# Kernel tuning notes

Hardware: AMD Instinct MI355X
Metric: run time of the kernel (lower is better)

## Reference

```python
import jax, jax.numpy as jnp
import numpy as np

WINDOW = (1, 7, 7)
DIM_HEAD = 32


def _rel_pos_index(ws):
    d, h, w = ws
    coords = np.stack(np.meshgrid(np.arange(d), np.arange(h), np.arange(w), indexing='ij'))
    cf = coords.reshape(3, -1)                      # [3, N]
    rel = (cf[:, :, None] - cf[:, None, :]).transpose(1, 2, 0).copy()  # [N, N, 3]
    rel[..., 0] += d - 1
    rel[..., 1] += h - 1
    rel[..., 2] += w - 1
    rel[..., 0] *= (2 * h - 1) * (2 * w - 1)
    rel[..., 1] *= (2 * w - 1)
    return jnp.asarray(rel.sum(-1))                 # [N, N] int32, N = 49


REL_IDX = _rel_pos_index(WINDOW)


def setup_inputs() -> dict:
    key = jax.random.key(0)
    k1, k2, k3, k4, k5 = jax.random.split(key, 5)
    B, X, Y, W1, W2, D = 4, 32, 32, 7, 7, 512
    heads = D // DIM_HEAD
    n_bias = (2 * WINDOW[0] - 1) * (2 * WINDOW[1] - 1) * (2 * WINDOW[2] - 1)  # 169
    s = 1.0 / np.sqrt(D)
    return {
        'x': jax.random.normal(k1, (B, X, Y, W1, W2, D), jnp.float32),
        'y': jax.random.normal(k2, (B, X, Y, W1, W2, D), jnp.float32),
        'Wq': jax.random.normal(k3, (D, D), jnp.float32) * s,
        'Wkv': jax.random.normal(k4, (D, 2 * D), jnp.float32) * s,
        'bias_table': jax.random.normal(k5, (n_bias, heads), jnp.float32) * 0.02,
    }


def reference(x, y, Wq, Wkv, bias_table):
    B, X, Y, W1, W2, D = x.shape
    h = D // DIM_HEAD
    n = W1 * W2                                     # 49 tokens per window
    scale = DIM_HEAD ** -0.5

    xr = x.reshape(B * X * Y, n, D)                 # [Bw, n, D]
    yr = y.reshape(B * X * Y, n, D)

    q = xr @ Wq                                     # [Bw, n, D]
    kv = yr @ Wkv                                   # [Bw, n, 2D]
    k, v = kv[..., :D], kv[..., D:]

    def to_heads(t):
        return t.reshape(t.shape[0], n, h, DIM_HEAD).transpose(0, 2, 1, 3)  # [Bw, h, n, dh]

    q, k, v = to_heads(q), to_heads(k), to_heads(v)

    sim = jnp.einsum('bhid,bhjd->bhij', q, k) * scale   # [Bw, h, n, n]
    bias = bias_table[REL_IDX]                          # [n, n, h]
    sim = sim + bias.transpose(2, 0, 1)[None]           # broadcast over windows

    attn = jax.nn.softmax(sim, axis=-1)
    out = jnp.einsum('bhij,bhjd->bhid', attn, v)        # [Bw, h, n, dh]
    out = out.transpose(0, 2, 1, 3).reshape(B * X * Y, W1, W2, D)
    return out.reshape(B, X, Y, W1, W2, D)
```

## Files before the change

kernel.cpp:

```cpp
#include <hip/hip_runtime.h>


typedef __bf16 bf16x8 __attribute__((ext_vector_type(8)));
typedef __attribute__((ext_vector_type(4))) float f32x4;

#define DEVI __device__ __forceinline__

DEVI unsigned short f2bf(float f) {
  union { float f; unsigned u; } v; v.f = f;
  unsigned r = v.u + 0x7FFFu + ((v.u >> 16) & 1u);
  return (unsigned short)(r >> 16);
}
DEVI unsigned pkbf(float a, float b) {
  return (unsigned)f2bf(a) | ((unsigned)f2bf(b) << 16);
}

#define MFMA16(a, b, c) __builtin_amdgcn_mfma_f32_16x16x32_bf16((a), (b), (c), 0, 0, 0)

#define SWZ_Y(r)  ((((unsigned)(r)) & 7u) << 4)
#define SWZ_A(r)  (((((unsigned)(r)) >> 2) & 3u) << 5)
#define SWZ_P(r)  ((((unsigned)(r)) & 7u) << 4)
#define SWZ_VT(r) ((((unsigned)(r)) & 7u) << 4)

__global__ void prep_kernel(const float* __restrict__ Wq, const float* __restrict__ Wkv,
                            const float* __restrict__ bt, char* __restrict__ ws) {
  int t = blockIdx.x * 256 + threadIdx.x;
  if (t < 786432) {
    int e = t & 7, lane = (t >> 3) & 63, ks = (t >> 9) & 15, nt = (t >> 13) & 1,
        h = (t >> 14) & 15, T = t >> 18;
    int row = ks * 32 + (lane >> 4) * 8 + e;
    int col = h * 32 + nt * 16 + (lane & 15);
    float v;
    if (T == 0)      v = Wq[row * 512 + col] * 0.17677669529663687f;
    else if (T == 1) v = Wkv[row * 1024 + col];
    else             v = Wkv[row * 1024 + 512 + col];
    ((unsigned short*)ws)[t] = f2bf(v);
  }
  if (t < 262144) {
    int r = t & 3, lane = (t >> 2) & 63, nt = (t >> 8) & 3, mt = (t >> 10) & 3,
        h = (t >> 12) & 15;
    int i = mt * 16 + (lane & 15);
    int j = nt * 16 + ((lane >> 4) & 3) * 4 + r;
    float v;
    if (j >= 49)      v = -1e30f;
    else if (i >= 49) v = 0.0f;
    else {
      int hi = i / 7, wi = i % 7, hj = j / 7, wj = j % 7;
      v = bt[((hi - hj + 6) * 13 + (wi - wj + 6)) * 16 + h];
    }
    ((float*)(ws + 1572864))[t] = v;
  }
}

DEVI bf16x8 ldXY(const char* base, int row, int kc) {
  unsigned a = ((unsigned)(row * 1024 + kc * 2)) ^ SWZ_Y(row);
  return *(const bf16x8*)(base + a);
}
DEVI bf16x8 ldXY_c(const char* base, int row, int kc) {
  int rc = row < 48 ? row : 48;
  bf16x8 v = ldXY(base, rc, kc);
  if (row > 48) {
    union { long long z[2]; bf16x8 v; } u; u.z[0] = 0; u.z[1] = 0;
    v = u.v;
  }
  return v;
}
DEVI bf16x8 ldA(const char* base, int row, int kc) {
  int rc = row < 48 ? row : 48;
  unsigned a = ((unsigned)(rc * 64 + kc * 2)) ^ SWZ_A(rc);
  return *(const bf16x8*)(base + a);
}
DEVI bf16x8 ldP2(const char* base, int row, int jc) {
  int rc = row < 48 ? row : 48;
  unsigned a = ((unsigned)(rc * 128 + jc * 2)) ^ SWZ_P(rc);
  return *(const bf16x8*)(base + a);
}
DEVI bf16x8 ldVT(const char* base, int dh, int jc) {
  unsigned a = ((unsigned)(dh * 128 + jc * 2)) ^ SWZ_VT(dh);
  return *(const bf16x8*)(base + a);
}

__global__ __launch_bounds__(512, 2)
void attn_kernel(const float* __restrict__ x, const float* __restrict__ y,
                 const char* __restrict__ wsW, const float* __restrict__ biasD,
                 float* __restrict__ out) {
  extern __shared__ char smem[];
  char* xb = smem;
  char* yb = smem + 50176;
  const int tid = threadIdx.x;
  const int lane = tid & 63, wave = tid >> 6;
  const int p = wave >> 1, sub = wave & 1;
  const int g = lane >> 4, lr = lane & 15;
  char* pbase = smem + 100352 + p * 15872;
  char* qAb = pbase;
  char* kbuf = pbase + 3136;
  char* qBb = pbase + 6272;
  char* vt = pbase + 9408;

  const int bw = blockIdx.x;
  const float* xs = x + (size_t)bw * 25088;
  const float* ys = y + (size_t)bw * 25088;

  for (int it = tid; it < 6272; it += 512) {
    float4 v = ((const float4*)xs)[it];
    float4 w = ((const float4*)ys)[it];
    int i = it >> 7;
    int k = (it & 127) << 2;
    unsigned a = ((unsigned)(i * 1024 + k * 2)) ^ SWZ_Y(i);
    uint2 ux, uy;
    ux.x = pkbf(v.x, v.y); ux.y = pkbf(v.z, v.w);
    uy.x = pkbf(w.x, w.y); uy.y = pkbf(w.z, w.w);
    *(uint2*)(xb + a) = ux;
    *(uint2*)(yb + a) = uy;
  }

  const bf16x8* wsQ = (const bf16x8*)wsW;
  const bf16x8* wsK = (const bf16x8*)(wsW + 524288);
  const bf16x8* wsV = (const bf16x8*)(wsW + 1048576);
  const f32x4* bD = (const f32x4*)biasD;
  const f32x4 fz = {0.f, 0.f, 0.f, 0.f};

  auto storeQK = [&](char* qb, f32x4 (&acc)[4]) {
    #pragma unroll
    for (int mt = 0; mt < 4; ++mt)
      #pragma unroll
      for (int r = 0; r < 4; ++r) {
        int row = mt * 16 + g * 4 + r;
        if (row < 49) {
          unsigned a = ((unsigned)(row * 64 + (sub * 16 + lr) * 2)) ^ SWZ_A(row);
          *(unsigned short*)(qb + a) = f2bf(acc[mt][r]);
        }
      }
  };

  auto kv_compute = [&](int h, f32x4 (&ak)[4], f32x4 (&av)[4]) {
    #pragma unroll
    for (int mt = 0; mt < 4; ++mt) { ak[mt] = fz; av[mt] = fz; }
    const bf16x8* pK = wsK + (size_t)((h * 2 + sub) * 16) * 64 + lane;
    const bf16x8* pV = wsV + (size_t)((h * 2 + sub) * 16) * 64 + lane;
    bf16x8 ksr[8], vsr[8];
    #pragma unroll
    for (int i = 0; i < 8; ++i) { ksr[i] = pK[i * 64]; vsr[i] = pV[i * 64]; }
    #pragma unroll
    for (int ks = 0; ks < 16; ++ks) {
      bf16x8 bk = ksr[ks & 7], bv = vsr[ks & 7];
      if (ks < 8) { ksr[ks & 7] = pK[(ks + 8) * 64]; vsr[ks & 7] = pV[(ks + 8) * 64]; }
      int kc = ks * 32 + g * 8;
      bf16x8 a0 = ldXY(yb, lr, kc);
      bf16x8 a1 = ldXY(yb, lr + 16, kc);
      bf16x8 a2 = ldXY(yb, lr + 32, kc);
      bf16x8 a3 = ldXY_c(yb, lr + 48, kc);
      ak[0] = MFMA16(a0, bk, ak[0]);
      ak[1] = MFMA16(a1, bk, ak[1]);
      ak[2] = MFMA16(a2, bk, ak[2]);
      ak[3] = MFMA16(a3, bk, ak[3]);
      av[0] = MFMA16(a0, bv, av[0]);
      av[1] = MFMA16(a1, bv, av[1]);
      av[2] = MFMA16(a2, bv, av[2]);
      av[3] = MFMA16(a3, bv, av[3]);
    }
  };

  auto kv_store = [&](f32x4 (&ak)[4], f32x4 (&av)[4]) {
    storeQK(kbuf, ak);
    #pragma unroll
    for (int mt = 0; mt < 4; ++mt) {
      int dh = sub * 16 + lr;
      int t0 = mt * 16 + g * 4;
      unsigned a = ((unsigned)(dh * 128 + t0 * 2)) ^ SWZ_VT(dh);
      uint2 pk;
      pk.x = pkbf(av[mt][0], av[mt][1]);
      pk.y = pkbf(av[mt][2], av[mt][3]);
      *(uint2*)(vt + a) = pk;
    }
  };

  auto attn_head = [&](int h, const char* qbuf, char* Pb) {
    f32x4 bias[2][4];
    #pragma unroll
    for (int mi = 0; mi < 2; ++mi)
      #pragma unroll
      for (int nt = 0; nt < 4; ++nt)
        bias[mi][nt] = bD[(size_t)(((h * 4 + sub * 2 + mi) * 4 + nt) * 64 + lane)];

    bf16x8 qa[2], kf[4];
    #pragma unroll
    for (int mi = 0; mi < 2; ++mi) qa[mi] = ldA(qbuf, sub * 32 + mi * 16 + lr, g * 8);
    #pragma unroll
    for (int nt = 0; nt < 4; ++nt) kf[nt] = ldA(kbuf, nt * 16 + lr, g * 8);

    f32x4 accs[2][4];
    #pragma unroll
    for (int mi = 0; mi < 2; ++mi)
      #pragma unroll
      for (int nt = 0; nt < 4; ++nt)
        accs[mi][nt] = MFMA16(kf[nt], qa[mi], fz);

    uint2 pks[2][4];
    #pragma unroll
    for (int mi = 0; mi < 2; ++mi) {
      f32x4 vals[4];
      #pragma unroll
      for (int nt = 0; nt < 4; ++nt) vals[nt] = accs[mi][nt] + bias[mi][nt];
      float m = vals[0][0];
      #pragma unroll
      for (int nt = 0; nt < 4; ++nt)
        #pragma unroll
        for (int r = 0; r < 4; ++r) m = fmaxf(m, vals[nt][r]);
      m = fmaxf(m, __shfl_xor(m, 16));
      m = fmaxf(m, __shfl_xor(m, 32));
      float s = 0.f;
      #pragma unroll
      for (int nt = 0; nt < 4; ++nt)
        #pragma unroll
        for (int r = 0; r < 4; ++r) {
          float pv = __expf(vals[nt][r] - m);
          vals[nt][r] = pv;
          s += pv;
        }
      s += __shfl_xor(s, 16);
      s += __shfl_xor(s, 32);
      float inv = 1.0f / s;
      #pragma unroll
      for (int nt = 0; nt < 4; ++nt) {
        pks[mi][nt].x = pkbf(vals[nt][0] * inv, vals[nt][1] * inv);
        pks[mi][nt].y = pkbf(vals[nt][2] * inv, vals[nt][3] * inv);
      }
    }

    __syncthreads();

    #pragma unroll
    for (int mi = 0; mi < 2; ++mi) {
      int i = sub * 32 + mi * 16 + lr;
      if (i < 49) {
        #pragma unroll
        for (int nt = 0; nt < 4; ++nt) {
          unsigned a = ((unsigned)(i * 128 + (nt * 16 + g * 4) * 2)) ^ SWZ_P(i);
          *(uint2*)(Pb + a) = pks[mi][nt];
        }
      }
    }

    f32x4 acco[2][2];
    acco[0][0] = fz; acco[0][1] = fz; acco[1][0] = fz; acco[1][1] = fz;
    #pragma unroll
    for (int ks = 0; ks < 2; ++ks) {
      int jc = ks * 32 + g * 8;
      bf16x8 av0 = ldVT(vt, lr, jc);
      bf16x8 av1 = ldVT(vt, lr + 16, jc);
      bf16x8 bp0 = ldP2(Pb, sub * 32 + lr, jc);
      bf16x8 bp1 = ldP2(Pb, sub * 32 + 16 + lr, jc);
      acco[0][0] = MFMA16(av0, bp0, acco[0][0]);
      acco[0][1] = MFMA16(av0, bp1, acco[0][1]);
      acco[1][0] = MFMA16(av1, bp0, acco[1][0]);
      acco[1][1] = MFMA16(av1, bp1, acco[1][1]);
    }

    float* ow = out + (size_t)bw * 25088 + h * 32;
    #pragma unroll
    for (int it = 0; it < 2; ++it) {
      int tok = sub * 32 + it * 16 + lr;
      if (tok < 49) {
        #pragma unroll
        for (int dt = 0; dt < 2; ++dt)
          *(f32x4*)(&ow[(size_t)tok * 512 + dt * 16 + g * 4]) = acco[dt][it];
      }
    }
  };

  for (int hp = 0; hp < 2; ++hp) {
    const int hA = p * 4 + hp * 2, hB = hA + 1;

    __syncthreads();

    f32x4 aqA[4], aqB[4];
    #pragma unroll
    for (int mt = 0; mt < 4; ++mt) { aqA[mt] = fz; aqB[mt] = fz; }
    {
      const bf16x8* pQA = wsQ + (size_t)((hA * 2 + sub) * 16) * 64 + lane;
      const bf16x8* pQB = wsQ + (size_t)((hB * 2 + sub) * 16) * 64 + lane;
      bf16x8 ra[8], rb[8];
      #pragma unroll
      for (int i = 0; i < 8; ++i) { ra[i] = pQA[i * 64]; rb[i] = pQB[i * 64]; }
      #pragma unroll
      for (int ks = 0; ks < 16; ++ks) {
        bf16x8 fa = ra[ks & 7], fb = rb[ks & 7];
        if (ks < 8) { ra[ks & 7] = pQA[(ks + 8) * 64]; rb[ks & 7] = pQB[(ks + 8) * 64]; }
        int kc = ks * 32 + g * 8;
        bf16x8 a0 = ldXY(xb, lr, kc);
        bf16x8 a1 = ldXY(xb, lr + 16, kc);
        bf16x8 a2 = ldXY(xb, lr + 32, kc);
        bf16x8 a3 = ldXY_c(xb, lr + 48, kc);
        aqA[0] = MFMA16(a0, fa, aqA[0]);
        aqA[1] = MFMA16(a1, fa, aqA[1]);
        aqA[2] = MFMA16(a2, fa, aqA[2]);
        aqA[3] = MFMA16(a3, fa, aqA[3]);
        aqB[0] = MFMA16(a0, fb, aqB[0]);
        aqB[1] = MFMA16(a1, fb, aqB[1]);
        aqB[2] = MFMA16(a2, fb, aqB[2]);
        aqB[3] = MFMA16(a3, fb, aqB[3]);
      }
    }
    storeQK(qAb, aqA);
    storeQK(qBb, aqB);

    {
      f32x4 ak[4], av[4];
      kv_compute(hA, ak, av);
      kv_store(ak, av);
    }

    __syncthreads();

    attn_head(hA, qAb, pbase);

    {
      f32x4 ak[4], av[4];
      kv_compute(hB, ak, av);
      __syncthreads();
      kv_store(ak, av);
    }

    __syncthreads();

    attn_head(hB, qBb, pbase + 3136);
  }
}

extern "C" void kernel_launch(void* const* d_in, const int* in_sizes, int n_in,
                              void* d_out, int out_size, void* d_ws, size_t ws_size,
                              hipStream_t stream) {
  (void)in_sizes; (void)n_in; (void)out_size; (void)ws_size;
  const float* x = (const float*)d_in[0];
  const float* y = (const float*)d_in[1];
  const float* Wq = (const float*)d_in[2];
  const float* Wkv = (const float*)d_in[3];
  const float* bt = (const float*)d_in[4];
  float* out = (float*)d_out;
  char* ws = (char*)d_ws;

  prep_kernel<<<3072, 256, 0, stream>>>(Wq, Wkv, bt, ws);

  (void)hipFuncSetAttribute((const void*)attn_kernel,
                            hipFuncAttributeMaxDynamicSharedMemorySize, 163840);
  attn_kernel<<<4096, 512, 163840, stream>>>(x, y, (const char*)ws,
                                             (const float*)(ws + 1572864), out);
}
```

Before: 843.2 us.

## Give each wave whole heads and pass Q, V, P through register shuffles

Work is reassigned so each of the eight waves owns two full heads, instead of a pair of waves splitting each head. Q, V and the softmax probabilities are transposed into MFMA operand layout with cross-lane shuffles, not written to and read back from shared memory. Only K goes through a small per-wave scratch area, so the per-head block-wide barriers become wave-local LDS waits and the shared-memory footprint shrinks. The cost is more shuffle instructions, more registers per wave (risking spills at 512 threads with 2 blocks per CU) and roughly twice the weight loads per wave.

```diff
diff --git a/kernel.cpp b/kernel.cpp
--- a/kernel.cpp
+++ b/kernel.cpp
@@ -16,11 +16,11 @@
 }
 
 #define MFMA16(a, b, c) __builtin_amdgcn_mfma_f32_16x16x32_bf16((a), (b), (c), 0, 0, 0)
+#define WAVE_DS_FENCE() do { asm volatile("s_waitcnt lgkmcnt(0)" ::: "memory"); \
+                             __builtin_amdgcn_sched_barrier(0); } while (0)
 
 #define SWZ_Y(r)  ((((unsigned)(r)) & 7u) << 4)
 #define SWZ_A(r)  (((((unsigned)(r)) >> 2) & 3u) << 5)
-#define SWZ_P(r)  ((((unsigned)(r)) & 7u) << 4)
-#define SWZ_VT(r) ((((unsigned)(r)) & 7u) << 4)
 
 __global__ void prep_kernel(const float* __restrict__ Wq, const float* __restrict__ Wkv,
                             const float* __restrict__ bt, char* __restrict__ ws) {
@@ -56,28 +56,32 @@
   unsigned a = ((unsigned)(row * 1024 + kc * 2)) ^ SWZ_Y(row);
   return *(const bf16x8*)(base + a);
 }
-DEVI bf16x8 ldXY_c(const char* base, int row, int kc) {
+DEVI bf16x8 ldXYc(const char* base, int row, int kc) {
   int rc = row < 48 ? row : 48;
-  bf16x8 v = ldXY(base, rc, kc);
-  if (row > 48) {
-    union { long long z[2]; bf16x8 v; } u; u.z[0] = 0; u.z[1] = 0;
-    v = u.v;
-  }
-  return v;
+  return ldXY(base, rc, kc);
 }
 DEVI bf16x8 ldA(const char* base, int row, int kc) {
   int rc = row < 48 ? row : 48;
   unsigned a = ((unsigned)(rc * 64 + kc * 2)) ^ SWZ_A(rc);
   return *(const bf16x8*)(base + a);
 }
-DEVI bf16x8 ldP2(const char* base, int row, int jc) {
-  int rc = row < 48 ? row : 48;
-  unsigned a = ((unsigned)(rc * 128 + jc * 2)) ^ SWZ_P(rc);
-  return *(const bf16x8*)(base + a);
-}
-DEVI bf16x8 ldVT(const char* base, int dh, int jc) {
-  unsigned a = ((unsigned)(dh * 128 + jc * 2)) ^ SWZ_VT(dh);
-  return *(const bf16x8*)(base + a);
+
+DEVI uint2 shfl_u2(uint2 v, int src) {
+  uint2 r;
+  r.x = (unsigned)__shfl((int)v.x, src);
+  r.y = (unsigned)__shfl((int)v.y, src);
+  return r;
+}
+DEVI bf16x8 xfrag(uint2 c0, uint2 c1, int srcA, int srcB, bool hig) {
+  uint2 a0 = shfl_u2(c0, srcA), a1 = shfl_u2(c1, srcA);
+  uint2 b0 = shfl_u2(c0, srcB), b1 = shfl_u2(c1, srcB);
+  uint2 lo = hig ? a1 : a0, hi = hig ? b1 : b0;
+  union { unsigned u[4]; bf16x8 v; } r;
+  r.u[0] = lo.x; r.u[1] = lo.y; r.u[2] = hi.x; r.u[3] = hi.y;
+  return r.v;
+}
+DEVI uint2 pk4(const f32x4& a) {
+  uint2 r; r.x = pkbf(a[0], a[1]); r.y = pkbf(a[2], a[3]); return r;
 }
 
 __global__ __launch_bounds__(512, 2)
@@ -89,13 +93,12 @@
   char* yb = smem + 50176;
   const int tid = threadIdx.x;
   const int lane = tid & 63, wave = tid >> 6;
-  const int p = wave >> 1, sub = wave & 1;
   const int g = lane >> 4, lr = lane & 15;
-  char* pbase = smem + 100352 + p * 15872;
-  char* qAb = pbase;
-  char* kbuf = pbase + 3136;
-  char* qBb = pbase + 6272;
-  char* vt = pbase + 9408;
+  char* kscr = smem + 100352 + wave * 3136;
+
+  const int srcA = lr + ((g & 1) << 5);
+  const int srcB = srcA + 16;
+  const bool hig = g >= 2;
 
   const int bw = blockIdx.x;
   const float* xs = x + (size_t)bw * 25088;
@@ -113,6 +116,7 @@
     *(uint2*)(xb + a) = ux;
     *(uint2*)(yb + a) = uy;
   }
+  __syncthreads();
 
   const bf16x8* wsQ = (const bf16x8*)wsW;
   const bf16x8* wsK = (const bf16x8*)(wsW + 524288);
@@ -120,211 +124,190 @@
   const f32x4* bD = (const f32x4*)biasD;
   const f32x4 fz = {0.f, 0.f, 0.f, 0.f};
 
-  auto storeQK = [&](char* qb, f32x4 (&acc)[4]) {
+  for (int hh = 0; hh < 2; ++hh) {
+    const int h = wave * 2 + hh;
+    WAVE_DS_FENCE();
+
+    f32x4 aQ[2][4];
+    #pragma unroll
+    for (int m = 0; m < 2; ++m)
+      #pragma unroll
+      for (int n = 0; n < 4; ++n) aQ[m][n] = fz;
+    {
+      const bf16x8* pQ0 = wsQ + (size_t)((h * 2 + 0) * 16) * 64 + lane;
+      const bf16x8* pQ1 = wsQ + (size_t)((h * 2 + 1) * 16) * 64 + lane;
+      bf16x8 ra[8], rb[8];
+      #pragma unroll
+      for (int i = 0; i < 8; ++i) { ra[i] = pQ0[i * 64]; rb[i] = pQ1[i * 64]; }
+      #pragma unroll
+      for (int ks = 0; ks < 16; ++ks) {
+        bf16x8 w0 = ra[ks & 7], w1 = rb[ks & 7];
+        if (ks < 8) { ra[ks & 7] = pQ0[(ks + 8) * 64]; rb[ks & 7] = pQ1[(ks + 8) * 64]; }
+        int kc = ks * 32 + g * 8;
+        bf16x8 b0 = ldXY(xb, lr, kc);
+        bf16x8 b1 = ldXY(xb, lr + 16, kc);
+        bf16x8 b2 = ldXY(xb, lr + 32, kc);
+        bf16x8 b3 = ldXYc(xb, lr + 48, kc);
+        aQ[0][0] = MFMA16(w0, b0, aQ[0][0]);
+        aQ[0][1] = MFMA16(w0, b1, aQ[0][1]);
+        aQ[0][2] = MFMA16(w0, b2, aQ[0][2]);
+        aQ[0][3] = MFMA16(w0, b3, aQ[0][3]);
+        aQ[1][0] = MFMA16(w1, b0, aQ[1][0]);
+        aQ[1][1] = MFMA16(w1, b1, aQ[1][1]);
+        aQ[1][2] = MFMA16(w1, b2, aQ[1][2]);
+        aQ[1][3] = MFMA16(w1, b3, aQ[1][3]);
+      }
+    }
+    uint2 pkQ[2][4];
+    #pragma unroll
+    for (int m = 0; m < 2; ++m)
+      #pragma unroll
+      for (int n = 0; n < 4; ++n) pkQ[m][n] = pk4(aQ[m][n]);
+
+    f32x4 aK[4][2], aV[4][2];
+    #pragma unroll
+    for (int mt = 0; mt < 4; ++mt) {
+      aK[mt][0] = fz; aK[mt][1] = fz; aV[mt][0] = fz; aV[mt][1] = fz;
+    }
+    {
+      const bf16x8* pK0 = wsK + (size_t)((h * 2 + 0) * 16) * 64 + lane;
+      const bf16x8* pK1 = wsK + (size_t)((h * 2 + 1) * 16) * 64 + lane;
+      const bf16x8* pV0 = wsV + (size_t)((h * 2 + 0) * 16) * 64 + lane;
+      const bf16x8* pV1 = wsV + (size_t)((h * 2 + 1) * 16) * 64 + lane;
+      bf16x8 rk0[4], rk1[4], rv0[4], rv1[4];
+      #pragma unroll
+      for (int i = 0; i < 4; ++i) {
+        rk0[i] = pK0[i * 64]; rk1[i] = pK1[i * 64];
+        rv0[i] = pV0[i * 64]; rv1[i] = pV1[i * 64];
+      }
+      #pragma unroll
+      for (int ks = 0; ks < 16; ++ks) {
+        bf16x8 k0 = rk0[ks & 3], k1 = rk1[ks & 3];
+        bf16x8 v0 = rv0[ks & 3], v1 = rv1[ks & 3];
+        if (ks < 12) {
+          rk0[ks & 3] = pK0[(ks + 4) * 64]; rk1[ks & 3] = pK1[(ks + 4) * 64];
+          rv0[ks & 3] = pV0[(ks + 4) * 64]; rv1[ks & 3] = pV1[(ks + 4) * 64];
+        }
+        int kc = ks * 32 + g * 8;
+        bf16x8 a0 = ldXY(yb, lr, kc);
+        bf16x8 a1 = ldXY(yb, lr + 16, kc);
+        bf16x8 a2 = ldXY(yb, lr + 32, kc);
+        bf16x8 a3 = ldXYc(yb, lr + 48, kc);
+        aK[0][0] = MFMA16(a0, k0, aK[0][0]);
+        aK[1][0] = MFMA16(a1, k0, aK[1][0]);
+        aK[2][0] = MFMA16(a2, k0, aK[2][0]);
+        aK[3][0] = MFMA16(a3, k0, aK[3][0]);
+        aK[0][1] = MFMA16(a0, k1, aK[0][1]);
+        aK[1][1] = MFMA16(a1, k1, aK[1][1]);
+        aK[2][1] = MFMA16(a2, k1, aK[2][1]);
+        aK[3][1] = MFMA16(a3, k1, aK[3][1]);
+        aV[0][0] = MFMA16(a0, v0, aV[0][0]);
+        aV[1][0] = MFMA16(a1, v0, aV[1][0]);
+        aV[2][0] = MFMA16(a2, v0, aV[2][0]);
+        aV[3][0] = MFMA16(a3, v0, aV[3][0]);
+        aV[0][1] = MFMA16(a0, v1, aV[0][1]);
+        aV[1][1] = MFMA16(a1, v1, aV[1][1]);
+        aV[2][1] = MFMA16(a2, v1, aV[2][1]);
+        aV[3][1] = MFMA16(a3, v1, aV[3][1]);
+      }
+    }
     #pragma unroll
     for (int mt = 0; mt < 4; ++mt)
       #pragma unroll
-      for (int r = 0; r < 4; ++r) {
-        int row = mt * 16 + g * 4 + r;
-        if (row < 49) {
-          unsigned a = ((unsigned)(row * 64 + (sub * 16 + lr) * 2)) ^ SWZ_A(row);
-          *(unsigned short*)(qb + a) = f2bf(acc[mt][r]);
+      for (int nt = 0; nt < 2; ++nt)
+        #pragma unroll
+        for (int r = 0; r < 4; ++r) {
+          int row = mt * 16 + g * 4 + r;
+          if (row < 49) {
+            unsigned a = ((unsigned)(row * 64 + (nt * 16 + lr) * 2)) ^ SWZ_A(row);
+            *(unsigned short*)(kscr + a) = f2bf(aK[mt][nt][r]);
+          }
         }
-      }
-  };
-
-  auto kv_compute = [&](int h, f32x4 (&ak)[4], f32x4 (&av)[4]) {
-    #pragma unroll
-    for (int mt = 0; mt < 4; ++mt) { ak[mt] = fz; av[mt] = fz; }
-    const bf16x8* pK = wsK + (size_t)((h * 2 + sub) * 16) * 64 + lane;
-    const bf16x8* pV = wsV + (size_t)((h * 2 + sub) * 16) * 64 + lane;
-    bf16x8 ksr[8], vsr[8];
-    #pragma unroll
-    for (int i = 0; i < 8; ++i) { ksr[i] = pK[i * 64]; vsr[i] = pV[i * 64]; }
-    #pragma unroll
-    for (int ks = 0; ks < 16; ++ks) {
-      bf16x8 bk = ksr[ks & 7], bv = vsr[ks & 7];
-      if (ks < 8) { ksr[ks & 7] = pK[(ks + 8) * 64]; vsr[ks & 7] = pV[(ks + 8) * 64]; }
-      int kc = ks * 32 + g * 8;
-      bf16x8 a0 = ldXY(yb, lr, kc);
-      bf16x8 a1 = ldXY(yb, lr + 16, kc);
-      bf16x8 a2 = ldXY(yb, lr + 32, kc);
-      bf16x8 a3 = ldXY_c(yb, lr + 48, kc);
-      ak[0] = MFMA16(a0, bk, ak[0]);
-      ak[1] = MFMA16(a1, bk, ak[1]);
-      ak[2] = MFMA16(a2, bk, ak[2]);
-      ak[3] = MFMA16(a3, bk, ak[3]);
-      av[0] = MFMA16(a0, bv, av[0]);
-      av[1] = MFMA16(a1, bv, av[1]);
-      av[2] = MFMA16(a2, bv, av[2]);
-      av[3] = MFMA16(a3, bv, av[3]);
-    }
-  };
-
-  auto kv_store = [&](f32x4 (&ak)[4], f32x4 (&av)[4]) {
-    storeQK(kbuf, ak);
+    uint2 pkV[4][2];
     #pragma unroll
     for (int mt = 0; mt < 4; ++mt) {
-      int dh = sub * 16 + lr;
-      int t0 = mt * 16 + g * 4;
-      unsigned a = ((unsigned)(dh * 128 + t0 * 2)) ^ SWZ_VT(dh);
-      uint2 pk;
-      pk.x = pkbf(av[mt][0], av[mt][1]);
-      pk.y = pkbf(av[mt][2], av[mt][3]);
-      *(uint2*)(vt + a) = pk;
-    }
-  };
-
-  auto attn_head = [&](int h, const char* qbuf, char* Pb) {
-    f32x4 bias[2][4];
-    #pragma unroll
-    for (int mi = 0; mi < 2; ++mi)
-      #pragma unroll
-      for (int nt = 0; nt < 4; ++nt)
-        bias[mi][nt] = bD[(size_t)(((h * 4 + sub * 2 + mi) * 4 + nt) * 64 + lane)];
-
-    bf16x8 qa[2], kf[4];
-    #pragma unroll
-    for (int mi = 0; mi < 2; ++mi) qa[mi] = ldA(qbuf, sub * 32 + mi * 16 + lr, g * 8);
-    #pragma unroll
-    for (int nt = 0; nt < 4; ++nt) kf[nt] = ldA(kbuf, nt * 16 + lr, g * 8);
-
-    f32x4 accs[2][4];
-    #pragma unroll
-    for (int mi = 0; mi < 2; ++mi)
-      #pragma unroll
-      for (int nt = 0; nt < 4; ++nt)
-        accs[mi][nt] = MFMA16(kf[nt], qa[mi], fz);
-
-    uint2 pks[2][4];
-    #pragma unroll
-    for (int mi = 0; mi < 2; ++mi) {
+      pkV[mt][0] = pk4(aV[mt][0]);
+      pkV[mt][1] = pk4(aV[mt][1]);
+    }
+    WAVE_DS_FENCE();
+    bf16x8 kf[4];
+    #pragma unroll
+    for (int jt = 0; jt < 4; ++jt) kf[jt] = ldA(kscr, jt * 16 + lr, g * 8);
+
+    uint2 pkP[4][4];
+    f32x4 bnext[4];
+    #pragma unroll
+    for (int jt = 0; jt < 4; ++jt)
+      bnext[jt] = bD[(size_t)(((h * 4 + 0) * 4 + jt) * 64 + lane)];
+    #pragma unroll
+    for (int it = 0; it < 4; ++it) {
+      f32x4 bs[4];
+      #pragma unroll
+      for (int jt = 0; jt < 4; ++jt) bs[jt] = bnext[jt];
+      if (it < 3) {
+        #pragma unroll
+        for (int jt = 0; jt < 4; ++jt)
+          bnext[jt] = bD[(size_t)(((h * 4 + it + 1) * 4 + jt) * 64 + lane)];
+      }
+      bf16x8 qf = xfrag(pkQ[0][it], pkQ[1][it], srcA, srcB, hig);
       f32x4 vals[4];
       #pragma unroll
-      for (int nt = 0; nt < 4; ++nt) vals[nt] = accs[mi][nt] + bias[mi][nt];
+      for (int jt = 0; jt < 4; ++jt) vals[jt] = MFMA16(kf[jt], qf, fz);
+      #pragma unroll
+      for (int jt = 0; jt < 4; ++jt) vals[jt] = vals[jt] + bs[jt];
       float m = vals[0][0];
       #pragma unroll
-      for (int nt = 0; nt < 4; ++nt)
-        #pragma unroll
-        for (int r = 0; r < 4; ++r) m = fmaxf(m, vals[nt][r]);
+      for (int jt = 0; jt < 4; ++jt)
+        #pragma unroll
+        for (int r = 0; r < 4; ++r) m = fmaxf(m, vals[jt][r]);
       m = fmaxf(m, __shfl_xor(m, 16));
       m = fmaxf(m, __shfl_xor(m, 32));
       float s = 0.f;
       #pragma unroll
-      for (int nt = 0; nt < 4; ++nt)
+      for (int jt = 0; jt < 4; ++jt)
         #pragma unroll
         for (int r = 0; r < 4; ++r) {
-          float pv = __expf(vals[nt][r] - m);
-          vals[nt][r] = pv;
+          float pv = __expf(vals[jt][r] - m);
+          vals[jt][r] = pv;
           s += pv;
         }
       s += __shfl_xor(s, 16);
       s += __shfl_xor(s, 32);
       float inv = 1.0f / s;
       #pragma unroll
-      for (int nt = 0; nt < 4; ++nt) {
-        pks[mi][nt].x = pkbf(vals[nt][0] * inv, vals[nt][1] * inv);
-        pks[mi][nt].y = pkbf(vals[nt][2] * inv, vals[nt][3] * inv);
-      }
-    }
-
-    __syncthreads();
-
-    #pragma unroll
-    for (int mi = 0; mi < 2; ++mi) {
-      int i = sub * 32 + mi * 16 + lr;
-      if (i < 49) {
-        #pragma unroll
-        for (int nt = 0; nt < 4; ++nt) {
-          unsigned a = ((unsigned)(i * 128 + (nt * 16 + g * 4) * 2)) ^ SWZ_P(i);
-          *(uint2*)(Pb + a) = pks[mi][nt];
-        }
-      }
-    }
-
-    f32x4 acco[2][2];
-    acco[0][0] = fz; acco[0][1] = fz; acco[1][0] = fz; acco[1][1] = fz;
+      for (int jt = 0; jt < 4; ++jt) {
+        pkP[it][jt].x = pkbf(vals[jt][0] * inv, vals[jt][1] * inv);
+        pkP[it][jt].y = pkbf(vals[jt][2] * inv, vals[jt][3] * inv);
+      }
+    }
+
+    f32x4 acco[2][4];
+    #pragma unroll
+    for (int md = 0; md < 2; ++md)
+      #pragma unroll
+      for (int it = 0; it < 4; ++it) acco[md][it] = fz;
     #pragma unroll
     for (int ks = 0; ks < 2; ++ks) {
-      int jc = ks * 32 + g * 8;
-      bf16x8 av0 = ldVT(vt, lr, jc);
-      bf16x8 av1 = ldVT(vt, lr + 16, jc);
-      bf16x8 bp0 = ldP2(Pb, sub * 32 + lr, jc);
-      bf16x8 bp1 = ldP2(Pb, sub * 32 + 16 + lr, jc);
-      acco[0][0] = MFMA16(av0, bp0, acco[0][0]);
-      acco[0][1] = MFMA16(av0, bp1, acco[0][1]);
-      acco[1][0] = MFMA16(av1, bp0, acco[1][0]);
-      acco[1][1] = MFMA16(av1, bp1, acco[1][1]);
+      bf16x8 aV0 = xfrag(pkV[ks * 2][0], pkV[ks * 2 + 1][0], srcA, srcB, hig);
+      bf16x8 aV1 = xfrag(pkV[ks * 2][1], pkV[ks * 2 + 1][1], srcA, srcB, hig);
+      #pragma unroll
+      for (int it = 0; it < 4; ++it) {
+        bf16x8 bP = xfrag(pkP[it][ks * 2], pkP[it][ks * 2 + 1], srcA, srcB, hig);
+        acco[0][it] = MFMA16(aV0, bP, acco[0][it]);
+        acco[1][it] = MFMA16(aV1, bP, acco[1][it]);
+      }
     }
 
     float* ow = out + (size_t)bw * 25088 + h * 32;
     #pragma unroll
-    for (int it = 0; it < 2; ++it) {
-      int tok = sub * 32 + it * 16 + lr;
+    for (int it = 0; it < 4; ++it) {
+      int tok = it * 16 + lr;
       if (tok < 49) {
         #pragma unroll
-        for (int dt = 0; dt < 2; ++dt)
-          *(f32x4*)(&ow[(size_t)tok * 512 + dt * 16 + g * 4]) = acco[dt][it];
-      }
-    }
-  };
-
-  for (int hp = 0; hp < 2; ++hp) {
-    const int hA = p * 4 + hp * 2, hB = hA + 1;
-
-    __syncthreads();
-
-    f32x4 aqA[4], aqB[4];
-    #pragma unroll
-    for (int mt = 0; mt < 4; ++mt) { aqA[mt] = fz; aqB[mt] = fz; }
-    {
-      const bf16x8* pQA = wsQ + (size_t)((hA * 2 + sub) * 16) * 64 + lane;
-      const bf16x8* pQB = wsQ + (size_t)((hB * 2 + sub) * 16) * 64 + lane;
-      bf16x8 ra[8], rb[8];
-      #pragma unroll
-      for (int i = 0; i < 8; ++i) { ra[i] = pQA[i * 64]; rb[i] = pQB[i * 64]; }
-      #pragma unroll
-      for (int ks = 0; ks < 16; ++ks) {
-        bf16x8 fa = ra[ks & 7], fb = rb[ks & 7];
-        if (ks < 8) { ra[ks & 7] = pQA[(ks + 8) * 64]; rb[ks & 7] = pQB[(ks + 8) * 64]; }
-        int kc = ks * 32 + g * 8;
-        bf16x8 a0 = ldXY(xb, lr, kc);
-        bf16x8 a1 = ldXY(xb, lr + 16, kc);
-        bf16x8 a2 = ldXY(xb, lr + 32, kc);
-        bf16x8 a3 = ldXY_c(xb, lr + 48, kc);
-        aqA[0] = MFMA16(a0, fa, aqA[0]);
-        aqA[1] = MFMA16(a1, fa, aqA[1]);
-        aqA[2] = MFMA16(a2, fa, aqA[2]);
-        aqA[3] = MFMA16(a3, fa, aqA[3]);
-        aqB[0] = MFMA16(a0, fb, aqB[0]);
-        aqB[1] = MFMA16(a1, fb, aqB[1]);
-        aqB[2] = MFMA16(a2, fb, aqB[2]);
-        aqB[3] = MFMA16(a3, fb, aqB[3]);
-      }
-    }
-    storeQK(qAb, aqA);
-    storeQK(qBb, aqB);
-
-    {
-      f32x4 ak[4], av[4];
-      kv_compute(hA, ak, av);
-      kv_store(ak, av);
-    }
-
-    __syncthreads();
-
-    attn_head(hA, qAb, pbase);
-
-    {
-      f32x4 ak[4], av[4];
-      kv_compute(hB, ak, av);
-      __syncthreads();
-      kv_store(ak, av);
-    }
-
-    __syncthreads();
-
-    attn_head(hB, qBb, pbase + 3136);
+        for (int md = 0; md < 2; ++md)
+          *(f32x4*)(&ow[(size_t)tok * 512 + md * 16 + g * 4]) = acco[md][it];
+      }
+    }
   }
 }
 
@@ -343,7 +326,7 @@
   prep_kernel<<<3072, 256, 0, stream>>>(Wq, Wkv, bt, ws);
 
   (void)hipFuncSetAttribute((const void*)attn_kernel,
-                            hipFuncAttributeMaxDynamicSharedMemorySize, 163840);
-  attn_kernel<<<4096, 512, 163840, stream>>>(x, y, (const char*)ws,
+                            hipFuncAttributeMaxDynamicSharedMemorySize, 125440);
+  attn_kernel<<<4096, 512, 125440, stream>>>(x, y, (const char*)ws,
                                              (const float*)(ws + 1572864), out);
 }
```

Result: slower. 1.048 ms (+24.3%).
